# Kernel tuning notes

Hardware: AMD Instinct MI355X
Metric: run time of the kernel (lower is better)

## Reference

```python
import jax, jax.numpy as jnp
import numpy as np

KH = KW = 2  # kernel_size
SH = SW = 2  # stride (== kernel, non-overlapping)

def setup_inputs() -> dict:
    key = jax.random.key(0)
    x = jax.random.normal(key, (64, 256, 112, 112), dtype=jnp.float32)
    return {"x": x}

def reference(x) -> jnp.ndarray:
    # Eval-mode stochastic pool: out = sum_k w_k * (w_k / sum_j w_j) over each
    # KHxKW window of relu(x); windows with zero sum produce 0.
    t = jax.nn.relu(x)
    B, C, H, W = t.shape
    Ho, Wo = H // SH, W // SW
    # stride == kernel -> non-overlapping windows via reshape (matches unfold)
    w = t.reshape(B, C, Ho, KH, Wo, KW).transpose(0, 1, 2, 4, 3, 5)
    w = w.reshape(B, C, Ho, Wo, KH * KW)
    s = w.sum(axis=-1)                      # [B,C,Ho,Wo]
    s_adj = jnp.where(s == 0, jnp.ones_like(s), s)
    out = (w * w).sum(axis=-1) / s_adj      # sum(w * w/sum(w))
    return out
```

## Files before the change

### kernel.cpp

```cpp
#include <hip/hip_runtime.h>


#define W_IN   112
#define WO     56
#define HO     56
#define WP     28
#define PLANE  (112 * 112)
#define OPLANE (56 * 56)

__global__ __launch_bounds__(256) void stoch_pool2d_kernel(
    const float* __restrict__ in, float* __restrict__ out, unsigned int npairs) {
    unsigned int stride = gridDim.x * blockDim.x;
    for (unsigned int p = blockIdx.x * blockDim.x + threadIdx.x; p < npairs;
         p += stride) {
        unsigned int wp   = p % WP;
        unsigned int rest = p / WP;
        unsigned int ho   = rest % HO;
        unsigned int bc   = rest / HO;

        unsigned int ibase = bc * PLANE + (2u * ho) * W_IN + wp * 4u;
        float4 r0 = *reinterpret_cast<const float4*>(in + ibase);
        float4 r1 = *reinterpret_cast<const float4*>(in + ibase + W_IN);

        float a0 = fmaxf(r0.x, 0.f), a1 = fmaxf(r0.y, 0.f);
        float a2 = fmaxf(r0.z, 0.f), a3 = fmaxf(r0.w, 0.f);
        float b0 = fmaxf(r1.x, 0.f), b1 = fmaxf(r1.y, 0.f);
        float b2 = fmaxf(r1.z, 0.f), b3 = fmaxf(r1.w, 0.f);

        float s0 = (a0 + a1) + (b0 + b1);
        float q0 = (a0 * a0 + a1 * a1) + (b0 * b0 + b1 * b1);
        float s1 = (a2 + a3) + (b2 + b3);
        float q1 = (a2 * a2 + a3 * a3) + (b2 * b2 + b3 * b3);

        float o0 = (s0 > 0.f) ? (q0 / s0) : 0.f;
        float o1 = (s1 > 0.f) ? (q1 / s1) : 0.f;

        unsigned int obase = bc * OPLANE + ho * WO + wp * 2u;
        *reinterpret_cast<float2*>(out + obase) = make_float2(o0, o1);
    }
}

extern "C" void kernel_launch(void* const* d_in, const int* in_sizes, int n_in,
                              void* d_out, int out_size, void* d_ws, size_t ws_size,
                              hipStream_t stream) {
    const float* x = (const float*)d_in[0];
    float* out = (float*)d_out;

    unsigned int npairs = (unsigned int)((long long)in_sizes[0] / 8);

    const int block = 256;
    const int grid = 2048;
    stoch_pool2d_kernel<<<grid, block, 0, stream>>>(x, out, npairs);
}
```

Baseline: 216.8 us.

## Stage contiguous input chunks through LDS with nontemporal loads and stores

Each block now processes 64-row chunks (7168 floats) of the input. The chunk is loaded fully coalesced as float4 with nontemporal hints and staged into shared memory. The 2x2 windows are then computed from LDS, and each thread writes one output element with a nontemporal store. Division is replaced with a hardware reciprocal approximation and the grid is resized. This adds shared-memory traffic, barriers and lower LDS occupancy, and it changes output stores from float2 to scalar.

```diff
diff --git a/kernel.cpp b/kernel.cpp
--- a/kernel.cpp
+++ b/kernel.cpp
@@ -1,42 +1,48 @@
 #include <hip/hip_runtime.h>
 
 
-#define W_IN   112
-#define WO     56
-#define HO     56
-#define WP     28
-#define PLANE  (112 * 112)
-#define OPLANE (56 * 56)
+typedef float v4f __attribute__((ext_vector_type(4)));
+typedef float v2f __attribute__((ext_vector_type(2)));
+
+#define NCHUNK 28672u
+#define CH_IN  7168u
+#define CH_OUT 1792u
 
 __global__ __launch_bounds__(256) void stoch_pool2d_kernel(
-    const float* __restrict__ in, float* __restrict__ out, unsigned int npairs) {
-    unsigned int stride = gridDim.x * blockDim.x;
-    for (unsigned int p = blockIdx.x * blockDim.x + threadIdx.x; p < npairs;
-         p += stride) {
-        unsigned int wp   = p % WP;
-        unsigned int rest = p / WP;
-        unsigned int ho   = rest % HO;
-        unsigned int bc   = rest / HO;
+    const float* __restrict__ in, float* __restrict__ out) {
+    __shared__ float lds[CH_IN];
+    const unsigned int t = threadIdx.x;
 
-        unsigned int ibase = bc * PLANE + (2u * ho) * W_IN + wp * 4u;
-        float4 r0 = *reinterpret_cast<const float4*>(in + ibase);
-        float4 r1 = *reinterpret_cast<const float4*>(in + ibase + W_IN);
+    for (unsigned int c = blockIdx.x; c < NCHUNK; c += gridDim.x) {
+        const v4f* src = reinterpret_cast<const v4f*>(in + (size_t)c * CH_IN);
 
-        float a0 = fmaxf(r0.x, 0.f), a1 = fmaxf(r0.y, 0.f);
-        float a2 = fmaxf(r0.z, 0.f), a3 = fmaxf(r0.w, 0.f);
-        float b0 = fmaxf(r1.x, 0.f), b1 = fmaxf(r1.y, 0.f);
-        float b2 = fmaxf(r1.z, 0.f), b3 = fmaxf(r1.w, 0.f);
+        v4f r[7];
+#pragma unroll
+        for (int i = 0; i < 7; ++i)
+            r[i] = __builtin_nontemporal_load(src + (i * 256u + t));
+#pragma unroll
+        for (int i = 0; i < 7; ++i)
+            reinterpret_cast<v4f*>(lds)[i * 256u + t] = r[i];
+        __syncthreads();
 
-        float s0 = (a0 + a1) + (b0 + b1);
-        float q0 = (a0 * a0 + a1 * a1) + (b0 * b0 + b1 * b1);
-        float s1 = (a2 + a3) + (b2 + b3);
-        float q1 = (a2 * a2 + a3 * a3) + (b2 * b2 + b3 * b3);
+        float* dst = out + (size_t)c * CH_OUT;
+        const v2f* l2 = reinterpret_cast<const v2f*>(lds);
+#pragma unroll
+        for (int i = 0; i < 7; ++i) {
+            unsigned int o    = i * 256u + t;
+            unsigned int orow = o / 56u;
+            unsigned int ocol = o - orow * 56u;
+            v2f top = l2[(2u * orow)      * 56u + ocol];
+            v2f bot = l2[(2u * orow + 1u) * 56u + ocol];
 
-        float o0 = (s0 > 0.f) ? (q0 / s0) : 0.f;
-        float o1 = (s1 > 0.f) ? (q1 / s1) : 0.f;
-
-        unsigned int obase = bc * OPLANE + ho * WO + wp * 2u;
-        *reinterpret_cast<float2*>(out + obase) = make_float2(o0, o1);
+            float a0 = fmaxf(top.x, 0.f), a1 = fmaxf(top.y, 0.f);
+            float b0 = fmaxf(bot.x, 0.f), b1 = fmaxf(bot.y, 0.f);
+            float s = (a0 + a1) + (b0 + b1);
+            float q = (a0 * a0 + a1 * a1) + (b0 * b0 + b1 * b1);
+            float v = (s > 0.f) ? q * __builtin_amdgcn_rcpf(s) : 0.f;
+            __builtin_nontemporal_store(v, dst + o);
+        }
+        __syncthreads();
     }
 }
 
@@ -46,9 +52,7 @@
     const float* x = (const float*)d_in[0];
     float* out = (float*)d_out;
 
-    unsigned int npairs = (unsigned int)((long long)in_sizes[0] / 8);
-
     const int block = 256;
-    const int grid = 2048;
-    stoch_pool2d_kernel<<<grid, block, 0, stream>>>(x, out, npairs);
+    const int grid = 2560;
+    stoch_pool2d_kernel<<<grid, block, 0, stream>>>(x, out);
 }
```

Result: faster. 186.7 us (-13.8%).

## Stream input contiguously per block with nontemporal loads and row-parity store masking

Applied to the files above, without the earlier changes.

Replaces the grid-stride pair mapping with fixed contiguous spans per block. Each lane loads a float4 and the float4 one input row below, and only lanes on even rows store their output, so reads are linear streams. Loads and stores use nontemporal hints, and the division becomes a hardware reciprocal multiply. The cost is that every input vector is fetched twice, once as the top row and once as the bottom row, and half the lanes' results are thrown away. Shapes are now hardcoded and the reciprocal is slightly less precise than a true division.

```diff
diff --git a/kernel.cpp b/kernel.cpp
--- a/kernel.cpp
+++ b/kernel.cpp
@@ -1,42 +1,62 @@
 #include <hip/hip_runtime.h>
 
 
-#define W_IN   112
-#define WO     56
-#define HO     56
-#define WP     28
-#define PLANE  (112 * 112)
-#define OPLANE (56 * 56)
+typedef float v4f __attribute__((ext_vector_type(4)));
+typedef float v2f __attribute__((ext_vector_type(2)));
+
+#define N4     51380224u
+#define NSPAN  802816u
+#define GRID   2048u
+#define SPB    392u
+#define WITERS 98u
+
+__device__ __forceinline__ v2f pool_pair(v4f A, v4f B) {
+    float a0 = fmaxf(A.x, 0.f), a1 = fmaxf(A.y, 0.f);
+    float a2 = fmaxf(A.z, 0.f), a3 = fmaxf(A.w, 0.f);
+    float b0 = fmaxf(B.x, 0.f), b1 = fmaxf(B.y, 0.f);
+    float b2 = fmaxf(B.z, 0.f), b3 = fmaxf(B.w, 0.f);
+    float s0 = (a0 + a1) + (b0 + b1);
+    float q0 = (a0 * a0 + a1 * a1) + (b0 * b0 + b1 * b1);
+    float s1 = (a2 + a3) + (b2 + b3);
+    float q1 = (a2 * a2 + a3 * a3) + (b2 * b2 + b3 * b3);
+    v2f o;
+    o.x = (s0 > 0.f) ? q0 * __builtin_amdgcn_rcpf(s0) : 0.f;
+    o.y = (s1 > 0.f) ? q1 * __builtin_amdgcn_rcpf(s1) : 0.f;
+    return o;
+}
 
 __global__ __launch_bounds__(256) void stoch_pool2d_kernel(
-    const float* __restrict__ in, float* __restrict__ out, unsigned int npairs) {
-    unsigned int stride = gridDim.x * blockDim.x;
-    for (unsigned int p = blockIdx.x * blockDim.x + threadIdx.x; p < npairs;
-         p += stride) {
-        unsigned int wp   = p % WP;
-        unsigned int rest = p / WP;
-        unsigned int ho   = rest % HO;
-        unsigned int bc   = rest / HO;
+    const float* __restrict__ in, float* __restrict__ out) {
+    const v4f* in4  = reinterpret_cast<const v4f*>(in);
+    v2f*       out2 = reinterpret_cast<v2f*>(out);
 
-        unsigned int ibase = bc * PLANE + (2u * ho) * W_IN + wp * 4u;
-        float4 r0 = *reinterpret_cast<const float4*>(in + ibase);
-        float4 r1 = *reinterpret_cast<const float4*>(in + ibase + W_IN);
+    unsigned int wave = threadIdx.x >> 6;
+    unsigned int lane = threadIdx.x & 63u;
+    unsigned int f = (blockIdx.x * SPB + wave) * 64u + lane;
 
-        float a0 = fmaxf(r0.x, 0.f), a1 = fmaxf(r0.y, 0.f);
-        float a2 = fmaxf(r0.z, 0.f), a3 = fmaxf(r0.w, 0.f);
-        float b0 = fmaxf(r1.x, 0.f), b1 = fmaxf(r1.y, 0.f);
-        float b2 = fmaxf(r1.z, 0.f), b3 = fmaxf(r1.w, 0.f);
+    for (unsigned int i = 0; i < WITERS; i += 2u) {
+        unsigned int f0 = f;
+        unsigned int f1 = f + 256u;
+        unsigned int fb0 = f0 + 28u; fb0 = (fb0 < N4) ? fb0 : (N4 - 1u);
+        unsigned int fb1 = f1 + 28u; fb1 = (fb1 < N4) ? fb1 : (N4 - 1u);
 
-        float s0 = (a0 + a1) + (b0 + b1);
-        float q0 = (a0 * a0 + a1 * a1) + (b0 * b0 + b1 * b1);
-        float s1 = (a2 + a3) + (b2 + b3);
-        float q1 = (a2 * a2 + a3 * a3) + (b2 * b2 + b3 * b3);
+        v4f A0 = __builtin_nontemporal_load(in4 + f0);
+        v4f B0 = __builtin_nontemporal_load(in4 + fb0);
+        v4f A1 = __builtin_nontemporal_load(in4 + f1);
+        v4f B1 = __builtin_nontemporal_load(in4 + fb1);
 
-        float o0 = (s0 > 0.f) ? (q0 / s0) : 0.f;
-        float o1 = (s1 > 0.f) ? (q1 / s1) : 0.f;
+        unsigned int r0 = f0 / 28u;  unsigned int k0 = f0 - r0 * 28u;
+        unsigned int r1 = f1 / 28u;  unsigned int k1 = f1 - r1 * 28u;
 
-        unsigned int obase = bc * OPLANE + ho * WO + wp * 2u;
-        *reinterpret_cast<float2*>(out + obase) = make_float2(o0, o1);
+        v2f o0 = pool_pair(A0, B0);
+        v2f o1 = pool_pair(A1, B1);
+
+        if (!(r0 & 1u))
+            __builtin_nontemporal_store(o0, out2 + ((r0 >> 1) * 28u + k0));
+        if (!(r1 & 1u))
+            __builtin_nontemporal_store(o1, out2 + ((r1 >> 1) * 28u + k1));
+
+        f += 512u;
     }
 }
 
@@ -46,9 +66,5 @@
     const float* x = (const float*)d_in[0];
     float* out = (float*)d_out;
 
-    unsigned int npairs = (unsigned int)((long long)in_sizes[0] / 8);
-
-    const int block = 256;
-    const int grid = 2048;
-    stoch_pool2d_kernel<<<grid, block, 0, stream>>>(x, out, npairs);
+    stoch_pool2d_kernel<<<GRID, 256, 0, stream>>>(x, out);
 }
```

Measured after the change: 266.1 us. 22.8% more time.
